# Kernel tuning notes

Hardware: AMD Instinct MI355X
Metric: run time of the kernel (lower is better)

Reference implementation:

```python
import jax, jax.numpy as jnp
import numpy as np

SIZE = 640
FPN_STRIDES = (8, 16, 32, 64, 128)
REG_MAX = 16
NUM_CLASSES = 80
TOPK = 45


def _build_anchors():
    pts, boxes, strides = [], [], []
    for s in FPN_STRIDES:
        h, w = SIZE // s, SIZE // s
        y, x = np.meshgrid(np.arange(h), np.arange(w), indexing='ij')
        yf = y.ravel().astype(np.float32)
        xf = x.ravel().astype(np.float32)
        pts.append(np.stack([(yf + 0.5) * s, (xf + 0.5) * s], -1))
        boxes.append(np.stack([yf * s, xf * s, (yf + 1) * s, (xf + 1) * s], -1))
        strides.append(np.full(h * w, s, np.float32))
    return (jnp.asarray(np.concatenate(pts), jnp.float32),
            jnp.asarray(np.concatenate(boxes), jnp.float32),
            jnp.asarray(np.concatenate(strides), jnp.float32))


ANCHOR_PTS, ANCHOR_BOXES, STRIDES = _build_anchors()
NUM_ANCHORS = ANCHOR_PTS.shape[0]  # 8525


def _iou(b1, b2):
    # elementwise IoU over trailing dim 4 in (y1, x1, y2, x2); axes are symmetric
    ty = jnp.maximum(b1[..., 0], b2[..., 0])
    tx = jnp.maximum(b1[..., 1], b2[..., 1])
    by = jnp.minimum(b1[..., 2], b2[..., 2])
    bx = jnp.minimum(b1[..., 3], b2[..., 3])
    inter = jnp.clip(by - ty, 0.0) * jnp.clip(bx - tx, 0.0)
    a1 = (b1[..., 2] - b1[..., 0]) * (b1[..., 3] - b1[..., 1])
    a2 = (b2[..., 2] - b2[..., 0]) * (b2[..., 3] - b2[..., 1])
    return inter / (a1 + a2 - inter)


def _assign_single(gt_cls, gt_bbox, pred_d):
    # gt_cls: (N,), gt_bbox: (N,4), pred_d: (4,A)
    A, N, C = NUM_ANCHORS, gt_bbox.shape[0], NUM_CLASSES
    pts, boxes, strides = ANCHOR_PTS, ANCHOR_BOXES, STRIDES
    centers = (gt_bbox[:, :2] + gt_bbox[:, 2:]) / 2
    dist = jnp.linalg.norm(centers[:, None, :] - pts[None, :, :], axis=-1)  # (N,A)
    _, k_ind = jax.lax.top_k(-dist, TOPK)  # (N,K) nearest anchors
    kb = boxes[k_ind]  # (N,K,4)
    Dg = _iou(gt_bbox[:, None, :], kb)  # (N,K)
    tg = Dg.mean(1) + Dg.std(1, ddof=1)  # torch .std() is unbiased
    ap = pts[k_ind]  # (N,K,2)
    inside = ((gt_bbox[:, None, 0] <= ap[..., 0]) & (ap[..., 0] <= gt_bbox[:, None, 2]) &
              (gt_bbox[:, None, 1] <= ap[..., 1]) & (ap[..., 1] <= gt_bbox[:, None, 3]))
    valid = (Dg >= tg[:, None]) & inside  # (N,K)
    n_idx = jnp.broadcast_to(jnp.arange(N, dtype=jnp.int32)[:, None], (N, TOPK))
    pri = jnp.where(valid, n_idx, -1).ravel()
    a_flat = k_ind.ravel()
    win_d = jnp.full((A,), -1, jnp.int32).at[a_flat].max(pri)
    wb = gt_bbox[jnp.clip(win_d, 0)]  # (A,4)
    gt_d = jnp.stack([(pts[:, 0] - wb[:, 0]) / strides,
                      (pts[:, 1] - wb[:, 1]) / strides,
                      (wb[:, 2] - pts[:, 0]) / strides,
                      (wb[:, 3] - pts[:, 1]) / strides], 0)  # (4,A) = [dtop,dleft,dbottom,dright]
    gt_dfl = jnp.where(win_d[None, :] >= 0, gt_d, jnp.inf)
    cls_pair = gt_cls.astype(jnp.int32)[n_idx]  # (N,K)
    ca = (cls_pair * A + k_ind).ravel()
    win_q = jnp.full((C * A,), -1, jnp.int32).at[ca].max(pri).reshape(C, A)
    gbq = gt_bbox[jnp.clip(win_q, 0)]  # (C,A,4)
    # _overlap_tlbr: decode(gt_d)*stride around anchor point, clamped -> clipped gt box
    box1 = jnp.clip(gbq, 0.0, float(SIZE))  # (C,A,4)
    rd = pred_d * strides[None, :]  # (4,A) raw offsets
    box2 = jnp.stack([jnp.clip(pts[:, 0] - rd[0], 0.0, float(SIZE)),
                      jnp.clip(pts[:, 1] - rd[1], 0.0, float(SIZE)),
                      jnp.clip(pts[:, 0] + rd[2], 0.0, float(SIZE)),
                      jnp.clip(pts[:, 1] + rd[3], 0.0, float(SIZE))], -1)  # (A,4)
    q = _iou(box1, box2[None, :, :])  # (C,A)
    gt_qfl = jnp.where(win_q >= 0, q, 0.0)
    return gt_qfl, gt_dfl


def setup_inputs() -> dict:
    key = jax.random.key(0)
    k1, k2, k3, k4 = jax.random.split(key, 4)
    B, N = 16, 64
    tl = jax.random.uniform(k1, (B, N, 2), jnp.float32, 0.0, SIZE - 64.0)
    wh = jax.random.uniform(k2, (B, N, 2), jnp.float32, 16.0, 256.0)
    br = jnp.minimum(tl + wh, float(SIZE))
    gt_bboxes = jnp.concatenate([tl, br], -1)  # (y1,x1,y2,x2)
    gt_clses = jax.random.randint(k3, (B, N), 0, NUM_CLASSES)
    pred_reg = jax.random.normal(k4, (B, 4, REG_MAX + 1, NUM_ANCHORS), jnp.float32)
    return {"gt_clses_batch": gt_clses, "gt_bboxes_batch": gt_bboxes,
            "pred_reg_batch": pred_reg}


def reference(gt_clses_batch, gt_bboxes_batch, pred_reg_batch):
    p = jax.nn.softmax(pred_reg_batch, axis=2)
    rng = jnp.arange(REG_MAX + 1, dtype=p.dtype).reshape(1, 1, -1, 1)
    pred_d = (p * rng).sum(2)  # (B,4,A) integral distribution -> expected offsets
    qfl, dfl = jax.vmap(_assign_single)(gt_clses_batch, gt_bboxes_batch, pred_d)
    return qfl, dfl, ANCHOR_PTS, STRIDES
```

## Files before the change

### kernel.cpp

```cpp
#include <hip/hip_runtime.h>
#include <math.h>
#include <float.h>

#define A_TOTAL 8525
#define NUM_B   16
#define NUM_N   64
#define NUM_C   80
#define K_TOP   45
#define SIZE_F  640.0f

#define UNASSIGNED_SENTINEL 1.0e30f

#define CUTOFF_KEY 0x43000000u
#define NBINS      2144
#define NBINS_PAD  2304
#define CAND_MAX   768

#define QFL_FLOATS  ((size_t)NUM_B * NUM_C * A_TOTAL)
#define QFL_VEC4    (QFL_FLOATS / 4)
#define MASK_WORDS  (NUM_B * A_TOTAL)
#define MASK_VEC4   ((MASK_WORDS * 2) / 4)

__device__ __forceinline__ void anchor_decode(int a, float& py, float& px, float& s,
                                              float& qy0, float& qx0, float& qy1, float& qx1) {
    int rel, w; float sf;
    if (a < 6400)      { rel = a;        w = 80; sf = 8.f;   }
    else if (a < 8000) { rel = a - 6400; w = 40; sf = 16.f;  }
    else if (a < 8400) { rel = a - 8000; w = 20; sf = 32.f;  }
    else if (a < 8500) { rel = a - 8400; w = 10; sf = 64.f;  }
    else               { rel = a - 8500; w = 5;  sf = 128.f; }
    int y = rel / w, x = rel - y * w;
    float yf = (float)y, xf = (float)x;
    py  = (yf + 0.5f) * sf;  px  = (xf + 0.5f) * sf;
    qy0 = yf * sf;           qx0 = xf * sf;
    qy1 = (yf + 1.f) * sf;   qx1 = (xf + 1.f) * sf;
    s = sf;
}

__device__ __forceinline__ unsigned int dist_key(int i, float cy, float cx) {
    float py, px, s, q0, q1, q2, q3;
    anchor_decode(i, py, px, s, q0, q1, q2, q3);
    float dy = __fadd_rn(cy, -py);
    float dx = __fadd_rn(cx, -px);
    float v = sqrtf(__fadd_rn(__fmul_rn(dy, dy), __fmul_rn(dx, dx)));
    return __float_as_uint(v);
}

__device__ __forceinline__ float iou_box(float ay0, float ax0, float ay1, float ax1,
                                         float by0, float bx0, float by1, float bx1) {
    float ty = fmaxf(ay0, by0), tx = fmaxf(ax0, bx0);
    float by = fminf(ay1, by1), bx = fminf(ax1, bx1);
    float ih = fmaxf(__fadd_rn(by, -ty), 0.f);
    float iw = fmaxf(__fadd_rn(bx, -tx), 0.f);
    float inter = __fmul_rn(ih, iw);
    float a1 = __fmul_rn(__fadd_rn(ay1, -ay0), __fadd_rn(ax1, -ax0));
    float a2 = __fmul_rn(__fadd_rn(by1, -by0), __fadd_rn(bx1, -bx0));
    return inter / __fadd_rn(__fadd_rn(a1, a2), -inter);
}

__global__ __launch_bounds__(256) void prep_kernel(float* __restrict__ qfl,
                                                   unsigned long long* __restrict__ mask,
                                                   float* __restrict__ opts,
                                                   float* __restrict__ ostr) {
    size_t gid = (size_t)blockIdx.x * 256 + threadIdx.x;
    size_t nthreads = (size_t)gridDim.x * 256;

    float4* q4 = (float4*)qfl;
    for (size_t i = gid; i < QFL_VEC4; i += nthreads)
        q4[i] = make_float4(0.f, 0.f, 0.f, 0.f);

    uint4* m4 = (uint4*)mask;
    for (size_t i = gid; i < MASK_VEC4; i += nthreads)
        m4[i] = make_uint4(0u, 0u, 0u, 0u);

    for (size_t a = gid; a < A_TOTAL; a += nthreads) {
        float py, px, s, q0, q1, q2, q3;
        anchor_decode((int)a, py, px, s, q0, q1, q2, q3);
        opts[2 * a]     = py;
        opts[2 * a + 1] = px;
        ostr[a]         = s;
    }
}

__global__ __launch_bounds__(256) void assign_kernel(const float* __restrict__ gt_bbox,
                                                     unsigned long long* __restrict__ mask) {
    __shared__ unsigned int hist[NBINS_PAD];
    __shared__ unsigned int wtot[4];
    __shared__ unsigned int cand_key[CAND_MAX];
    __shared__ int          cand_idx[CAND_MAX];
    __shared__ int          s_candn;
    __shared__ int          s_B;
    __shared__ int          sel[K_TOP];
    __shared__ float        dg[K_TOP];
    __shared__ float        s_tg;

    int tid = threadIdx.x;
    int lane = tid & 63, wid = tid >> 6;
    int b = blockIdx.x >> 6;
    int n = blockIdx.x & 63;
    const float* gb = gt_bbox + (size_t)(b * NUM_N + n) * 4;
    float g0 = gb[0], g1 = gb[1], g2 = gb[2], g3 = gb[3];
    float cy = __fmul_rn(__fadd_rn(g0, g2), 0.5f);
    float cx = __fmul_rn(__fadd_rn(g1, g3), 0.5f);

    for (int i = tid; i < NBINS_PAD; i += 256) hist[i] = 0u;
    if (tid == 0) s_candn = 0;
    __syncthreads();

    for (int i = tid; i < A_TOTAL; i += 256) {
        unsigned int key = dist_key(i, cy, cx);
        if (key < CUTOFF_KEY) atomicAdd(&hist[key >> 19], 1u);
    }
    __syncthreads();

    unsigned int psum = 0;
    int base = tid * 9;
#pragma unroll
    for (int k = 0; k < 9; ++k) psum += hist[base + k];
    unsigned int x = psum;
    for (int off = 1; off < 64; off <<= 1) {
        unsigned int y = __shfl_up(x, off, 64);
        if (lane >= off) x += y;
    }
    if (lane == 63) wtot[wid] = x;
    __syncthreads();
    unsigned int wbase = 0;
    for (int w = 0; w < 4; ++w) wbase += (w < wid) ? wtot[w] : 0u;
    unsigned int inc = wbase + x;
    unsigned int exc = inc - psum;
    if (exc < (unsigned)K_TOP && inc >= (unsigned)K_TOP) {
        unsigned int cum = exc;
        int bbin = base;
        while (cum + hist[bbin] < (unsigned)K_TOP) { cum += hist[bbin]; ++bbin; }
        s_B = bbin;
    }
    __syncthreads();

    int B = s_B;
    for (int i = tid; i < A_TOTAL; i += 256) {
        unsigned int key = dist_key(i, cy, cx);
        if (key < CUTOFF_KEY && (int)(key >> 19) <= B) {
            int pos = atomicAdd(&s_candn, 1);
            if (pos < CAND_MAX) { cand_key[pos] = key; cand_idx[pos] = i; }
        }
    }
    __syncthreads();

    int M = s_candn < CAND_MAX ? s_candn : CAND_MAX;
    for (int i = tid; i < M; i += 256) {
        unsigned int ki = cand_key[i]; int ii = cand_idx[i];
        int rank = 0;
        for (int j = 0; j < M; ++j) {
            unsigned int kj = cand_key[j]; int ij = cand_idx[j];
            rank += (kj < ki || (kj == ki && ij < ii)) ? 1 : 0;
        }
        if (rank < K_TOP) sel[rank] = ii;
    }
    __syncthreads();

    if (tid < K_TOP) {
        int a = sel[tid];
        float py, px, s, q0, q1, q2, q3;
        anchor_decode(a, py, px, s, q0, q1, q2, q3);
        dg[tid] = iou_box(g0, g1, g2, g3, q0, q1, q2, q3);
    }
    __syncthreads();
    if (tid == 0) {
        float sum = 0.f;
        for (int k = 0; k < K_TOP; ++k) sum = __fadd_rn(sum, dg[k]);
        float mean = sum / (float)K_TOP;
        float ss = 0.f;
        for (int k = 0; k < K_TOP; ++k) {
            float d = __fadd_rn(dg[k], -mean);
            ss = __fadd_rn(ss, __fmul_rn(d, d));
        }
        s_tg = __fadd_rn(mean, sqrtf(ss / (float)(K_TOP - 1)));
    }
    __syncthreads();
    if (tid < K_TOP) {
        int a = sel[tid];
        float py, px, s, q0, q1, q2, q3;
        anchor_decode(a, py, px, s, q0, q1, q2, q3);
        bool inside = (g0 <= py) && (py <= g2) && (g1 <= px) && (px <= g3);
        if (inside && dg[tid] >= s_tg) {
            atomicOr(&mask[(size_t)b * A_TOTAL + a], 1ull << n);
        }
    }
}

__global__ __launch_bounds__(256) void output_kernel(const int* __restrict__ gt_cls,
                                                     const float* __restrict__ gt_bbox,
                                                     const float* __restrict__ pred_reg,
                                                     const unsigned long long* __restrict__ mask,
                                                     float* __restrict__ qfl,
                                                     float* __restrict__ dfl) {
    __shared__ float s_gb[NUM_N * 4];
    __shared__ float s_gc[NUM_N * 4];
    __shared__ int   s_cls[NUM_N];

    int tid = threadIdx.x;
    int b = blockIdx.y;
    if (tid < NUM_N * 4) {
        float v = gt_bbox[(size_t)b * NUM_N * 4 + tid];
        s_gb[tid] = v;
        s_gc[tid] = fminf(fmaxf(v, 0.f), SIZE_F);
    }
    if (tid < NUM_N) s_cls[tid] = gt_cls[b * NUM_N + tid];
    __syncthreads();

    int a = blockIdx.x * 256 + tid;
    if (a >= A_TOTAL) return;

    unsigned long long m64 = mask[(size_t)b * A_TOTAL + a];
    float* dflp = dfl + (size_t)b * 4 * A_TOTAL + a;

    if (m64 == 0ull) {
        dflp[0]           = UNASSIGNED_SENTINEL;
        dflp[A_TOTAL]     = UNASSIGNED_SENTINEL;
        dflp[2 * A_TOTAL] = UNASSIGNED_SENTINEL;
        dflp[3 * A_TOTAL] = UNASSIGNED_SENTINEL;
        return;
    }

    float py, px, s, q0, q1, q2, q3;
    anchor_decode(a, py, px, s, q0, q1, q2, q3);

    float rd[4];
    const float* pr = pred_reg + (size_t)b * 4 * 17 * A_TOTAL + a;
#pragma unroll
    for (int d = 0; d < 4; ++d) {
        float xv[17];
#pragma unroll
        for (int j = 0; j < 17; ++j) xv[j] = pr[(size_t)(d * 17 + j) * A_TOTAL];
        float m = xv[0];
#pragma unroll
        for (int j = 1; j < 17; ++j) m = fmaxf(m, xv[j]);
        float S = 0.f, dot = 0.f;
#pragma unroll
        for (int j = 0; j < 17; ++j) {
            float t = __expf(xv[j] - m);
            S += t;
            dot += t * (float)j;
        }
        rd[d] = (dot / S) * s;
    }
    float b2y0 = fminf(fmaxf(py - rd[0], 0.f), SIZE_F);
    float b2x0 = fminf(fmaxf(px - rd[1], 0.f), SIZE_F);
    float b2y1 = fminf(fmaxf(py + rd[2], 0.f), SIZE_F);
    float b2x1 = fminf(fmaxf(px + rd[3], 0.f), SIZE_F);

    {
        int n = 63 - __clzll(m64);
        dflp[0]            = (py - s_gb[n * 4 + 0]) / s;
        dflp[A_TOTAL]      = (px - s_gb[n * 4 + 1]) / s;
        dflp[2 * A_TOTAL]  = (s_gb[n * 4 + 2] - py) / s;
        dflp[3 * A_TOTAL]  = (s_gb[n * 4 + 3] - px) / s;
    }

    float* qflp = qfl + (size_t)b * NUM_C * A_TOTAL + a;
    unsigned long long seen0 = 0ull, seen1 = 0ull;
    unsigned long long mm = m64;
    while (mm) {
        int n = 63 - __clzll(mm);
        mm &= ~(1ull << n);
        int c = s_cls[n];
        bool done;
        if (c < 64) {
            unsigned long long bit = 1ull << c;
            done = (seen0 & bit) != 0ull; seen0 |= bit;
        } else {
            unsigned long long bit = 1ull << (c - 64);
            done = (seen1 & bit) != 0ull; seen1 |= bit;
        }
        if (!done) {
            qflp[(size_t)c * A_TOTAL] = iou_box(s_gc[n * 4 + 0], s_gc[n * 4 + 1],
                                                s_gc[n * 4 + 2], s_gc[n * 4 + 3],
                                                b2y0, b2x0, b2y1, b2x1);
        }
    }
}

extern "C" void kernel_launch(void* const* d_in, const int* in_sizes, int n_in,
                              void* d_out, int out_size, void* d_ws, size_t ws_size,
                              hipStream_t stream) {
    const int*   gt_cls   = (const int*)d_in[0];
    const float* gt_bbox  = (const float*)d_in[1];
    const float* pred_reg = (const float*)d_in[2];

    float* qfl  = (float*)d_out;
    float* dfl  = qfl + QFL_FLOATS;
    float* opts = dfl + (size_t)NUM_B * 4 * A_TOTAL;
    float* ostr = opts + (size_t)A_TOTAL * 2;

    unsigned long long* mask = (unsigned long long*)d_ws;

    hipLaunchKernelGGL(prep_kernel, dim3(2048), dim3(256), 0, stream, qfl, mask, opts, ostr);
    hipLaunchKernelGGL(assign_kernel, dim3(NUM_B * NUM_N), dim3(256), 0, stream, gt_bbox, mask);
    hipLaunchKernelGGL(output_kernel, dim3((A_TOTAL + 255) / 256, NUM_B), dim3(256), 0, stream,
                       gt_cls, gt_bbox, pred_reg, mask, qfl, dfl);
}
```

Baseline: 131.5 us.

## Restrict anchor scan to local windows and zero qfl in output kernel

```diff
diff --git a/kernel.cpp b/kernel.cpp
--- a/kernel.cpp
+++ b/kernel.cpp
@@ -12,12 +12,10 @@
 #define UNASSIGNED_SENTINEL 1.0e30f
 
 #define CUTOFF_KEY 0x43000000u
-#define NBINS      2144
 #define NBINS_PAD  2304
 #define CAND_MAX   768
 
 #define QFL_FLOATS  ((size_t)NUM_B * NUM_C * A_TOTAL)
-#define QFL_VEC4    (QFL_FLOATS / 4)
 #define MASK_WORDS  (NUM_B * A_TOTAL)
 #define MASK_VEC4   ((MASK_WORDS * 2) / 4)
 
@@ -37,9 +35,10 @@
     s = sf;
 }
 
-__device__ __forceinline__ unsigned int dist_key(int i, float cy, float cx) {
-    float py, px, s, q0, q1, q2, q3;
-    anchor_decode(i, py, px, s, q0, q1, q2, q3);
+__device__ __forceinline__ unsigned int dist_key_yx(int yy, int xx, float s,
+                                                    float cy, float cx) {
+    float py = __fmul_rn(__fadd_rn((float)yy, 0.5f), s);
+    float px = __fmul_rn(__fadd_rn((float)xx, 0.5f), s);
     float dy = __fadd_rn(cy, -py);
     float dx = __fadd_rn(cx, -px);
     float v = sqrtf(__fadd_rn(__fmul_rn(dy, dy), __fmul_rn(dx, dx)));
@@ -58,16 +57,11 @@
     return inter / __fadd_rn(__fadd_rn(a1, a2), -inter);
 }
 
-__global__ __launch_bounds__(256) void prep_kernel(float* __restrict__ qfl,
-                                                   unsigned long long* __restrict__ mask,
+__global__ __launch_bounds__(256) void prep_kernel(unsigned long long* __restrict__ mask,
                                                    float* __restrict__ opts,
                                                    float* __restrict__ ostr) {
     size_t gid = (size_t)blockIdx.x * 256 + threadIdx.x;
     size_t nthreads = (size_t)gridDim.x * 256;
-
-    float4* q4 = (float4*)qfl;
-    for (size_t i = gid; i < QFL_VEC4; i += nthreads)
-        q4[i] = make_float4(0.f, 0.f, 0.f, 0.f);
 
     uint4* m4 = (uint4*)mask;
     for (size_t i = gid; i < MASK_VEC4; i += nthreads)
@@ -94,6 +88,10 @@
     __shared__ float        dg[K_TOP];
     __shared__ float        s_tg;
 
+    const int   LH[5] = {80, 40, 20, 10, 5};
+    const int   LB[5] = {0, 6400, 8000, 8400, 8500};
+    const float LS[5] = {8.f, 16.f, 32.f, 64.f, 128.f};
+
     int tid = threadIdx.x;
     int lane = tid & 63, wid = tid >> 6;
     int b = blockIdx.x >> 6;
@@ -103,13 +101,31 @@
     float cy = __fmul_rn(__fadd_rn(g0, g2), 0.5f);
     float cx = __fmul_rn(__fadd_rn(g1, g3), 0.5f);
 
+    int wy0[5], wx0[5], wnc[5], wcl[5];
+#pragma unroll
+    for (int l = 0; l < 5; ++l) {
+        float s = LS[l]; int H = LH[l];
+        int y0 = (int)((cy - 68.f) / s) - 1; if (y0 < 0) y0 = 0;
+        int y1 = (int)((cy + 68.f) / s) + 1; if (y1 > H - 1) y1 = H - 1;
+        int x0 = (int)((cx - 68.f) / s) - 1; if (x0 < 0) x0 = 0;
+        int x1 = (int)((cx + 68.f) / s) + 1; if (x1 > H - 1) x1 = H - 1;
+        wy0[l] = y0; wx0[l] = x0;
+        wnc[l] = x1 - x0 + 1;
+        wcl[l] = (y1 - y0 + 1) * wnc[l];
+    }
+
     for (int i = tid; i < NBINS_PAD; i += 256) hist[i] = 0u;
     if (tid == 0) s_candn = 0;
     __syncthreads();
 
-    for (int i = tid; i < A_TOTAL; i += 256) {
-        unsigned int key = dist_key(i, cy, cx);
-        if (key < CUTOFF_KEY) atomicAdd(&hist[key >> 19], 1u);
+#pragma unroll
+    for (int l = 0; l < 5; ++l) {
+        int nc = wnc[l], cells = wcl[l];
+        for (int t = tid; t < cells; t += 256) {
+            int r = t / nc, c = t - r * nc;
+            unsigned int key = dist_key_yx(wy0[l] + r, wx0[l] + c, LS[l], cy, cx);
+            if (key < CUTOFF_KEY) atomicAdd(&hist[key >> 19], 1u);
+        }
     }
     __syncthreads();
 
@@ -137,11 +153,20 @@
     __syncthreads();
 
     int B = s_B;
-    for (int i = tid; i < A_TOTAL; i += 256) {
-        unsigned int key = dist_key(i, cy, cx);
-        if (key < CUTOFF_KEY && (int)(key >> 19) <= B) {
-            int pos = atomicAdd(&s_candn, 1);
-            if (pos < CAND_MAX) { cand_key[pos] = key; cand_idx[pos] = i; }
+#pragma unroll
+    for (int l = 0; l < 5; ++l) {
+        int nc = wnc[l], cells = wcl[l];
+        for (int t = tid; t < cells; t += 256) {
+            int r = t / nc, c = t - r * nc;
+            int yy = wy0[l] + r, xx = wx0[l] + c;
+            unsigned int key = dist_key_yx(yy, xx, LS[l], cy, cx);
+            if (key < CUTOFF_KEY && (int)(key >> 19) <= B) {
+                int pos = atomicAdd(&s_candn, 1);
+                if (pos < CAND_MAX) {
+                    cand_key[pos] = key;
+                    cand_idx[pos] = LB[l] + yy * LH[l] + xx;
+                }
+            }
         }
     }
     __syncthreads();
@@ -213,6 +238,10 @@
 
     unsigned long long m64 = mask[(size_t)b * A_TOTAL + a];
     float* dflp = dfl + (size_t)b * 4 * A_TOTAL + a;
+    float* qflp = qfl + (size_t)b * NUM_C * A_TOTAL + a;
+
+#pragma unroll
+    for (int c = 0; c < NUM_C; ++c) qflp[(size_t)c * A_TOTAL] = 0.f;
 
     if (m64 == 0ull) {
         dflp[0]           = UNASSIGNED_SENTINEL;
@@ -257,7 +286,6 @@
         dflp[3 * A_TOTAL]  = (s_gb[n * 4 + 3] - px) / s;
     }
 
-    float* qflp = qfl + (size_t)b * NUM_C * A_TOTAL + a;
     unsigned long long seen0 = 0ull, seen1 = 0ull;
     unsigned long long mm = m64;
     while (mm) {
@@ -294,7 +322,7 @@
 
     unsigned long long* mask = (unsigned long long*)d_ws;
 
-    hipLaunchKernelGGL(prep_kernel, dim3(2048), dim3(256), 0, stream, qfl, mask, opts, ostr);
+    hipLaunchKernelGGL(prep_kernel, dim3(256), dim3(256), 0, stream, mask, opts, ostr);
     hipLaunchKernelGGL(assign_kernel, dim3(NUM_B * NUM_N), dim3(256), 0, stream, gt_bbox, mask);
     hipLaunchKernelGGL(output_kernel, dim3((A_TOTAL + 255) / 256, NUM_B), dim3(256), 0, stream,
                        gt_cls, gt_bbox, pred_reg, mask, qfl, dfl);
```

Result: faster. 113.7 us (-13.5%).
